# Kernel optimization log

Measured on AMD Instinct MI355X. Metric: run time of the kernel, lower is better.

Reference implementation:

```python
import jax, jax.numpy as jnp
import numpy as np


def _shift(w):
    # max(0, -min(w)): scalar shift making w + shift non-negative
    return jnp.maximum(0.0, -jnp.min(w))


def shifted_linear(x, W, b=None):
    # F.linear with non-negative weights plus row-sum correction
    alpha = _shift(W)
    y = x @ (W + alpha).T - alpha * jnp.sum(x, axis=-1, keepdims=True)
    if b is not None:
        y = y + b
    return y


def shifted_depthwise_conv(x, w, b):
    # x: (B, D, L), w: (D, 1, K) depthwise; causal-style padding K-1, sliced to L by caller
    alpha = _shift(w)
    k = w.shape[2]
    pad = k - 1
    dn = ('NCH', 'OIH', 'NCH')
    groups = w.shape[0]
    y = jax.lax.conv_general_dilated(x, w + alpha, (1,), [(pad, pad)],
                                     dimension_numbers=dn, feature_group_count=groups)
    ones_k = jnp.ones_like(w)
    ssum = jax.lax.conv_general_dilated(x, ones_k, (1,), [(pad, pad)],
                                        dimension_numbers=dn, feature_group_count=groups)
    return y - alpha * ssum + b[None, :, None]


def setup_inputs() -> dict:
    key = jax.random.key(0)
    ks = jax.random.split(key, 10)
    d_model, d_inner, d_state, d_conv, dt_rank = 1024, 2048, 16, 4, 64
    B, L = 2, 1024
    s = 0.05
    return {
        'hidden_states': jax.random.normal(ks[0], (B, L, d_model), jnp.float32),
        'W_in': jax.random.normal(ks[1], (2 * d_inner, d_model), jnp.float32) * s,
        'conv_w': jax.random.normal(ks[2], (d_inner, 1, d_conv), jnp.float32) * 0.3,
        'conv_b': jax.random.normal(ks[3], (d_inner,), jnp.float32) * s,
        'W_x': jax.random.normal(ks[4], (dt_rank + 2 * d_state, d_inner), jnp.float32) * s,
        'W_dt': jax.random.normal(ks[5], (d_inner, dt_rank), jnp.float32) * s,
        'dt_bias': jax.random.normal(ks[6], (d_inner,), jnp.float32),
        'W_out': jax.random.normal(ks[7], (d_model, d_inner), jnp.float32) * s,
        'A_log': jax.random.normal(ks[8], (d_inner, d_state), jnp.float32) * 0.5,
        'D': jax.random.normal(ks[9], (d_inner,), jnp.float32),
    }


def reference(hidden_states, W_in, conv_w, conv_b, W_x, W_dt, dt_bias, W_out, A_log, D):
    b, l, dm = hidden_states.shape
    d_inner = conv_w.shape[0]
    d_state = A_log.shape[1]
    dt_rank = W_dt.shape[1]

    A = jnp.exp(A_log)  # (d_inner, d_state), always positive

    # in_proj over (b*l, d_model) -> (b, 2*d_inner, l)
    xz = shifted_linear(hidden_states.reshape(b * l, dm), W_in)
    xz = xz.reshape(b, l, 2 * d_inner).transpose(0, 2, 1)
    x, z = xz[:, :d_inner], xz[:, d_inner:]

    # depthwise shifted conv + SiLU activation, truncated to seqlen
    x = jax.nn.silu(shifted_depthwise_conv(x, conv_w, conv_b)[..., :l])

    # x_proj -> dt_raw, B, C
    x_dbl = shifted_linear(x.transpose(0, 2, 1).reshape(b * l, d_inner), W_x)
    dt_raw = x_dbl[:, :dt_rank]
    Bm = x_dbl[:, dt_rank:dt_rank + d_state].reshape(b, l, d_state).transpose(0, 2, 1)  # (b,n,l)
    Cm = x_dbl[:, dt_rank + d_state:].reshape(b, l, d_state).transpose(0, 2, 1)         # (b,n,l)
    dt = shifted_linear(dt_raw, W_dt).reshape(b, l, d_inner).transpose(0, 2, 1)          # (b,d,l)

    # delta activation (softplus) with bias, clamped
    delta = jnp.clip(jax.nn.softplus(dt + dt_bias[None, :, None]), 1e-4, 20.0)

    # global scalar shifts for B and C
    beta = _shift(Bm)
    gamma = _shift(Cm)
    B_nn = Bm + beta
    C_nn = Cm + gamma

    # precomputed per-step operands, scan axis first: (l, b, d, n)
    deltaA = jnp.exp(-jnp.einsum('bdl,dn->lbdn', delta, A))
    dBu = jnp.einsum('bdl,bnl,bdl->lbdn', delta, B_nn, x)
    C_scan = C_nn.transpose(2, 0, 1)  # (l, b, n)

    def step(xc, inp):
        dA_i, dBu_i, C_i = inp
        xc = dA_i * xc + dBu_i                                   # (b,d,n)
        y = jnp.einsum('bdn,bn->bd', xc, C_i) - gamma * jnp.sum(xc, axis=-1)
        return xc, y

    x0 = jnp.zeros((b, d_inner, d_state), dtype=delta.dtype)
    _, ys = jax.lax.scan(step, x0, (deltaA, dBu, C_scan))        # ys: (l, b, d)

    y = ys.transpose(1, 2, 0) + x * D[None, :, None]             # (b, d, l) skip term
    y = y * jax.nn.silu(z)                                       # gate activation

    out = shifted_linear(y.transpose(0, 2, 1).reshape(b * l, d_inner), W_out)
    return out.reshape(b, l, dm)
```

## Files before the change

### kernel.cpp

```cpp
#include <hip/hip_runtime.h>
#include <hip/hip_bf16.h>
#include <math.h>

#define DM 1024
#define DI 2048
#define DS 16
#define DTR 64
#define NB 2
#define LL 1024
#define TT (NB*LL)
#define SCH 32
#define NCH (LL/SCH)
#define KPLANES 8

typedef unsigned short u16;
typedef __attribute__((ext_vector_type(8))) short bf16x8;
typedef __attribute__((ext_vector_type(4))) float f32x4;

#define LOG2E 1.4426950408889634f

__device__ inline u16 f2bf(float f) {
  union { float f; unsigned u; } c; c.f = f;
  unsigned u = c.u;
  return (u16)((u + 0x7fffu + ((u >> 16) & 1u)) >> 16);
}
__device__ inline float bf2f(u16 u) {
  union { unsigned u; float f; } c; c.u = ((unsigned)u) << 16;
  return c.f;
}

__device__ inline unsigned fkey(float f) {
  union { float f; unsigned u; } c; c.f = f;
  return (c.u & 0x80000000u) ? ~c.u : (c.u | 0x80000000u);
}
__device__ inline float funkey(unsigned k) {
  union { unsigned u; float f; } c;
  c.u = (k & 0x80000000u) ? (k & 0x7fffffffu) : ~k;
  return c.f;
}

#define GLDS16(g, l) __builtin_amdgcn_global_load_lds( \
    (const __attribute__((address_space(1))) unsigned int*)(g), \
    (__attribute__((address_space(3))) unsigned int*)(l), 16, 0, 0)

template<int BM, int BN, int EPI, int OB>
__global__ __launch_bounds__(256) void gemm_bf16(
    const u16* __restrict__ A, const u16* __restrict__ B,
    void* __restrict__ Cv, int M, int N, int K, int kpb,
    const float* __restrict__ bias) {
  constexpr int WAVES_M = BM / 64;
  constexpr int WAVES_N = 4 / WAVES_M;
  constexpr int WTM = 4;
  constexpr int WTN = BN / (WAVES_N * 16);
  constexpr int ASLABS = BM / 16;
  constexpr int SLABS = (BM + BN) / 16;
  constexpr int SPW = SLABS / 4;
  __shared__ u16 As[BM * 32];
  __shared__ u16 Bs[BN * 32];
  const int tid = threadIdx.x;
  const int wave = tid >> 6;
  const int lane = tid & 63;
  const int bm = blockIdx.y * BM;
  const int bn = blockIdx.x * BN;
  const int wm = (wave / WAVES_N) * 64;
  const int wn = (wave % WAVES_N) * (WTN * 16);
  const int r4 = lane >> 2;
  const int kc = (lane & 3) * 8;
  const int fr = lane & 15;
  const int fq = lane >> 4;
  const int koff = blockIdx.z * kpb;
  float* C = (float*)Cv + (size_t)blockIdx.z * M * N;
  u16* C16 = (u16*)Cv;

  f32x4 acc[WTM][WTN];
#pragma unroll
  for (int i = 0; i < WTM; ++i)
#pragma unroll
    for (int j = 0; j < WTN; ++j) acc[i][j] = (f32x4){0.f, 0.f, 0.f, 0.f};

  for (int k0 = koff; k0 < koff + kpb; k0 += 32) {
#pragma unroll
    for (int s = wave * SPW; s < (wave + 1) * SPW; ++s) {
      if (s < ASLABS) {
        int row = s * 16 + r4;
        GLDS16(A + (size_t)(bm + row) * K + k0 + kc, &As[s * 512]);
      } else {
        int row = (s - ASLABS) * 16 + r4;
        GLDS16(B + (size_t)(bn + row) * K + k0 + kc, &Bs[(s - ASLABS) * 512]);
      }
    }
    __syncthreads();
    bf16x8 af[WTM], bf[WTN];
#pragma unroll
    for (int i = 0; i < WTM; ++i)
      af[i] = *(const bf16x8*)&As[(wm + 16 * i + fr) * 32 + fq * 8];
#pragma unroll
    for (int j = 0; j < WTN; ++j)
      bf[j] = *(const bf16x8*)&Bs[(wn + 16 * j + fr) * 32 + fq * 8];
#pragma unroll
    for (int i = 0; i < WTM; ++i)
#pragma unroll
      for (int j = 0; j < WTN; ++j)
        acc[i][j] = __builtin_amdgcn_mfma_f32_16x16x32_bf16(af[i], bf[j], acc[i][j], 0, 0, 0);
    __syncthreads();
  }

#pragma unroll
  for (int i = 0; i < WTM; ++i) {
    int row0 = bm + wm + 16 * i + fq * 4;
#pragma unroll
    for (int j = 0; j < WTN; ++j) {
      int col = bn + wn + 16 * j + fr;
#pragma unroll
      for (int r = 0; r < 4; ++r) {
        float v = acc[i][j][r];
        if (EPI == 1) {
          v += bias[col];
          float sp = (v > 20.0f) ? v : log1pf(expf(v));
          v = fminf(fmaxf(sp, 1e-4f), 20.0f);
        }
        if (OB == 1) C16[(size_t)(row0 + r) * N + col] = f2bf(v);
        else         C[(size_t)(row0 + r) * N + col] = v;
      }
    }
  }
}

__global__ __launch_bounds__(256) void gemm3_reduce(
    const float* __restrict__ part, float* __restrict__ xdb,
    u16* __restrict__ dtraw_bf, unsigned* __restrict__ betakey) {
  int i = blockIdx.x * 256 + threadIdx.x;
  int t = i >> 7, col = i & 127;
  float s = 0.f;
#pragma unroll
  for (int z = 0; z < KPLANES; ++z) s += part[(size_t)z * TT * 128 + i];
  if (col < 96) xdb[t * 96 + col] = s;
  if (col < 64) dtraw_bf[t * 64 + col] = f2bf(s);
  float mn = (col >= 64 && col < 80) ? s : 3.4e38f;
#pragma unroll
  for (int o = 32; o; o >>= 1) mn = fminf(mn, __shfl_down(mn, o));
  __shared__ float sm[4];
  if ((threadIdx.x & 63) == 0) sm[threadIdx.x >> 6] = mn;
  __syncthreads();
  if (threadIdx.x == 0) {
    float m = fminf(fminf(sm[0], sm[1]), fminf(sm[2], sm[3]));
    atomicMin(betakey, fkey(m));
  }
}

__global__ __launch_bounds__(256) void cast_all(
    const float* __restrict__ hs, const float* __restrict__ win,
    const float* __restrict__ wout, const float* __restrict__ wx,
    const float* __restrict__ wdt,
    u16* __restrict__ hs_bf, u16* __restrict__ win_bf,
    u16* __restrict__ wout_bf, u16* __restrict__ wx_bf,
    u16* __restrict__ wdt_bf, unsigned* __restrict__ betakey) {
  int gid = blockIdx.x * 256 + threadIdx.x;
  if (gid == 0) betakey[0] = 0xFFFFFFFFu;
  const float* src; u16* dst; int off;
  if (gid < 524288)       { src = hs;   dst = hs_bf;   off = gid; }
  else if (gid < 1572864) { src = win;  dst = win_bf;  off = gid - 524288; }
  else if (gid < 2097152) { src = wout; dst = wout_bf; off = gid - 1572864; }
  else if (gid < 2146304) { src = wx;   dst = wx_bf;   off = gid - 2097152; }
  else if (gid < 2179072) { src = wdt;  dst = wdt_bf;  off = gid - 2146304; }
  else {
    ushort4 z4 = {0, 0, 0, 0};
    ((ushort4*)wx_bf)[49152 + gid - 2179072] = z4;
    return;
  }
  float4 v = ((const float4*)src)[off];
  ushort4 o;
  o.x = f2bf(v.x); o.y = f2bf(v.y); o.z = f2bf(v.z); o.w = f2bf(v.w);
  ((ushort4*)dst)[off] = o;
}

__global__ __launch_bounds__(256) void conv_silu4(
    const u16* __restrict__ xz, const float* __restrict__ w,
    const float* __restrict__ cb, u16* __restrict__ xc_bf) {
  int gid = blockIdx.x * 256 + threadIdx.x;
  int dq = (gid & 511) * 4;
  int t = gid >> 9;
  int l = t & (LL - 1);
  float wv[4][4];
#pragma unroll
  for (int j = 0; j < 4; ++j) {
    float4 ww = *(const float4*)&w[(dq + j) * 4];
    wv[j][0] = ww.x; wv[j][1] = ww.y; wv[j][2] = ww.z; wv[j][3] = ww.w;
  }
  float4 acc = *(const float4*)&cb[dq];
#pragma unroll
  for (int k = 0; k < 4; ++k) {
    int ll = l - 3 + k;
    if (ll < 0) continue;
    ushort4 xv = *(const ushort4*)&xz[(size_t)(t - 3 + k) * (2 * DI) + dq];
    acc.x += bf2f(xv.x) * wv[0][k]; acc.y += bf2f(xv.y) * wv[1][k];
    acc.z += bf2f(xv.z) * wv[2][k]; acc.w += bf2f(xv.w) * wv[3][k];
  }
  acc.x /= (1.0f + expf(-acc.x)); acc.y /= (1.0f + expf(-acc.y));
  acc.z /= (1.0f + expf(-acc.z)); acc.w /= (1.0f + expf(-acc.w));
  ushort4 o;
  o.x = f2bf(acc.x); o.y = f2bf(acc.y); o.z = f2bf(acc.z); o.w = f2bf(acc.w);
  *(ushort4*)&xc_bf[(size_t)t * DI + dq] = o;
}

__global__ __launch_bounds__(256) void scan_pass1(
    const u16* __restrict__ delta, const u16* __restrict__ xc_bf,
    const float* __restrict__ xdb, const float* __restrict__ A_log,
    const unsigned* __restrict__ betak,
    float* __restrict__ hend, float* __restrict__ Ssum) {
  const int d = blockIdx.x * 256 + threadIdx.x;
  const int c = blockIdx.y;
  const int b = blockIdx.z;
  __shared__ float Bsh[SCH][16];
  const float beta = fmaxf(0.0f, -funkey(betak[0]));
  const int t0 = b * LL + c * SCH;
  for (int i = threadIdx.x; i < SCH * 16; i += 256) {
    int tt = i >> 4, n = i & 15;
    Bsh[tt][n] = xdb[(size_t)(t0 + tt) * 96 + 64 + n] + beta;
  }
  __syncthreads();
  float Av2[16];
#pragma unroll
  for (int n = 0; n < 16; ++n) Av2[n] = expf(A_log[d * 16 + n]) * LOG2E;
  float h[16];
#pragma unroll
  for (int n = 0; n < 16; ++n) h[n] = 0.f;
  float S = 0.f;
  for (int tt = 0; tt < SCH; ++tt) {
    int t = t0 + tt;
    float dv = bf2f(delta[(size_t)t * DI + d]);
    float xv = bf2f(xc_bf[(size_t)t * DI + d]);
    float dx = dv * xv;
    S += dv;
#pragma unroll
    for (int n = 0; n < 16; ++n) {
      float a = __builtin_amdgcn_exp2f(-dv * Av2[n]);
      h[n] = a * h[n] + dx * Bsh[tt][n];
    }
  }
  size_t base = (((size_t)(b * NCH + c) * DI) + d) * 16;
#pragma unroll
  for (int n = 0; n < 16; ++n) hend[base + n] = h[n];
  Ssum[((size_t)(b * NCH + c) * DI) + d] = S;
}

__global__ __launch_bounds__(256) void scan_pass2(
    float* __restrict__ hend, const float* __restrict__ Ssum,
    const float* __restrict__ A_log) {
  int gid = blockIdx.x * 256 + threadIdx.x;
  int n = gid & 15;
  int d = (gid >> 4) & (DI - 1);
  int b = gid >> 15;
  float Av2 = expf(A_log[d * 16 + n]) * LOG2E;
  float H = 0.f;
  for (int c = 0; c < NCH; ++c) {
    size_t cb = ((size_t)(b * NCH + c) * DI) + d;
    float hl = hend[cb * 16 + n];
    float p = __builtin_amdgcn_exp2f(-Av2 * Ssum[cb]);
    hend[cb * 16 + n] = H;
    H = p * H + hl;
  }
}

__global__ __launch_bounds__(256) void scan_pass3(
    const u16* __restrict__ delta, const u16* __restrict__ xc_bf,
    const float* __restrict__ xdb, const u16* __restrict__ xz_bf,
    const float* __restrict__ A_log, const float* __restrict__ Dp,
    const unsigned* __restrict__ betak, const float* __restrict__ hstart,
    u16* __restrict__ ybf) {
  const int d = blockIdx.x * 256 + threadIdx.x;
  const int c = blockIdx.y;
  const int b = blockIdx.z;
  __shared__ float Bsh[SCH][16];
  __shared__ float Csh[SCH][16];
  const float beta = fmaxf(0.0f, -funkey(betak[0]));
  const int t0 = b * LL + c * SCH;
  for (int i = threadIdx.x; i < SCH * 16; i += 256) {
    int tt = i >> 4, n = i & 15;
    size_t row = (size_t)(t0 + tt) * 96;
    Bsh[tt][n] = xdb[row + 64 + n] + beta;
    Csh[tt][n] = xdb[row + 80 + n];
  }
  __syncthreads();
  float Av2[16];
#pragma unroll
  for (int n = 0; n < 16; ++n) Av2[n] = expf(A_log[d * 16 + n]) * LOG2E;
  float h[16];
  size_t base = (((size_t)(b * NCH + c) * DI) + d) * 16;
#pragma unroll
  for (int n = 0; n < 16; ++n) h[n] = hstart[base + n];
  const float Dd = Dp[d];
  for (int tt = 0; tt < SCH; ++tt) {
    int t = t0 + tt;
    float dv = bf2f(delta[(size_t)t * DI + d]);
    float xv = bf2f(xc_bf[(size_t)t * DI + d]);
    float dx = dv * xv;
    float yv = 0.f;
#pragma unroll
    for (int n = 0; n < 16; ++n) {
      float a = __builtin_amdgcn_exp2f(-dv * Av2[n]);
      h[n] = a * h[n] + dx * Bsh[tt][n];
      yv += h[n] * Csh[tt][n];
    }
    float zv = bf2f(xz_bf[(size_t)t * (2 * DI) + DI + d]);
    float out = (yv + xv * Dd) * (zv / (1.0f + expf(-zv)));
    ybf[(size_t)t * DI + d] = f2bf(out);
  }
}

extern "C" void kernel_launch(void* const* d_in, const int* in_sizes, int n_in,
                              void* d_out, int out_size, void* d_ws, size_t ws_size,
                              hipStream_t stream) {
  const float* hs      = (const float*)d_in[0];
  const float* W_in    = (const float*)d_in[1];
  const float* conv_w  = (const float*)d_in[2];
  const float* conv_b  = (const float*)d_in[3];
  const float* W_x     = (const float*)d_in[4];
  const float* W_dt    = (const float*)d_in[5];
  const float* dt_bias = (const float*)d_in[6];
  const float* W_out   = (const float*)d_in[7];
  const float* A_log   = (const float*)d_in[8];
  const float* Dp      = (const float*)d_in[9];
  float* out = (float*)d_out;

  float* ws       = (float*)d_ws;
  float* xz_bfR   = ws;
  float* xcv_bfR  = xz_bfR + (size_t)TT * 2 * DI / 2;
  float* xdb      = xcv_bfR + (size_t)TT * DI / 2;
  float* dlt_bfR  = xdb + (size_t)TT * 96;
  float* part     = dlt_bfR + (size_t)TT * DI / 2;
  float* betab    = part + (size_t)KPLANES * TT * 128;
  float* hend     = betab + 64;
  float* Ssum     = hend + (size_t)NB * NCH * DI * 16;
  float* hs_bfR   = Ssum + (size_t)NB * NCH * DI;
  float* win_bfR  = hs_bfR + (size_t)TT * DM / 2;
  float* wout_bfR = win_bfR + (size_t)2 * DI * DM / 2;
  float* wx_bfR   = wout_bfR + (size_t)DM * DI / 2;
  float* wdt_bfR  = wx_bfR + 131072;
  float* dtraw_bfR = wdt_bfR + 65536;

  u16* xz_bf    = (u16*)xz_bfR;
  u16* xcv_bf   = (u16*)xcv_bfR;
  u16* dlt_bf   = (u16*)dlt_bfR;
  u16* hs_bf    = (u16*)hs_bfR;
  u16* win_bf   = (u16*)win_bfR;
  u16* wout_bf  = (u16*)wout_bfR;
  u16* wx_bf    = (u16*)wx_bfR;
  u16* wdt_bf   = (u16*)wdt_bfR;
  u16* dtraw_bf = (u16*)dtraw_bfR;
  unsigned* betakey = (unsigned*)betab;
  u16* ybf      = (u16*)win_bfR;

  dim3 blk(256);

  cast_all<<<8576, blk, 0, stream>>>(hs, W_in, W_out, W_x, W_dt,
                                     hs_bf, win_bf, wout_bf, wx_bf, wdt_bf,
                                     betakey);

  gemm_bf16<128, 64, 0, 1><<<dim3(4096 / 64, TT / 128), blk, 0, stream>>>(
      hs_bf, win_bf, xz_bf, TT, 2 * DI, DM, DM, nullptr);

  conv_silu4<<<(TT * DI / 4) / 256, blk, 0, stream>>>(xz_bf, conv_w, conv_b, xcv_bf);

  gemm_bf16<64, 128, 0, 0><<<dim3(1, TT / 64, KPLANES), blk, 0, stream>>>(
      xcv_bf, wx_bf, part, TT, 128, DI, DI / KPLANES, nullptr);
  gemm3_reduce<<<1024, blk, 0, stream>>>(part, xdb, dtraw_bf, betakey);

  gemm_bf16<64, 128, 1, 1><<<dim3(DI / 128, TT / 64), blk, 0, stream>>>(
      dtraw_bf, wdt_bf, dlt_bf, TT, DI, DTR, DTR, dt_bias);

  scan_pass1<<<dim3(DI / 256, NCH, NB), blk, 0, stream>>>(
      dlt_bf, xcv_bf, xdb, A_log, betakey, hend, Ssum);
  scan_pass2<<<(NB * DI * DS) / 256, blk, 0, stream>>>(hend, Ssum, A_log);
  scan_pass3<<<dim3(DI / 256, NCH, NB), blk, 0, stream>>>(
      dlt_bf, xcv_bf, xdb, xz_bf, A_log, Dp, betakey, hend, ybf);

  gemm_bf16<64, 64, 0, 0><<<dim3(DM / 64, TT / 64), blk, 0, stream>>>(
      ybf, wout_bf, out, TT, DM, DI, DI, nullptr);
}
```

Baseline: 270.5 us.

## Replace split-K partial buffers with atomic accumulation and enlarge GEMM tiles

The x_proj split-K GEMM now atomically adds into a zeroed xdb buffer, which removes the partial-plane buffer and its reduce kernel. A small dtbeta kernel replaces the reduce and handles the dt bf16 cast and the beta min. The in_proj GEMM moves to 128x128 tiles. The out_proj GEMM becomes a 4-way split-K with 128x128 tiles that atomically accumulates into the output, which cast_all now zeroes. The atomics add contention, make float summation order nondeterministic, and cut the number of blocks for in_proj.

```diff
diff --git a/kernel.cpp b/kernel.cpp
--- a/kernel.cpp
+++ b/kernel.cpp
@@ -11,7 +11,6 @@
 #define TT (NB*LL)
 #define SCH 32
 #define NCH (LL/SCH)
-#define KPLANES 8
 
 typedef unsigned short u16;
 typedef __attribute__((ext_vector_type(8))) short bf16x8;
@@ -43,7 +42,7 @@
     (const __attribute__((address_space(1))) unsigned int*)(g), \
     (__attribute__((address_space(3))) unsigned int*)(l), 16, 0, 0)
 
-template<int BM, int BN, int EPI, int OB>
+template<int BM, int BN, int EPI, int OB, int CG = 0>
 __global__ __launch_bounds__(256) void gemm_bf16(
     const u16* __restrict__ A, const u16* __restrict__ B,
     void* __restrict__ Cv, int M, int N, int K, int kpb,
@@ -69,7 +68,7 @@
   const int fr = lane & 15;
   const int fq = lane >> 4;
   const int koff = blockIdx.z * kpb;
-  float* C = (float*)Cv + (size_t)blockIdx.z * M * N;
+  float* C = (float*)Cv + (OB == 0 ? (size_t)blockIdx.z * M * N : (size_t)0);
   u16* C16 = (u16*)Cv;
 
   f32x4 acc[WTM][WTN];
@@ -119,30 +118,43 @@
           float sp = (v > 20.0f) ? v : log1pf(expf(v));
           v = fminf(fmaxf(sp, 1e-4f), 20.0f);
         }
-        if (OB == 1) C16[(size_t)(row0 + r) * N + col] = f2bf(v);
-        else         C[(size_t)(row0 + r) * N + col] = v;
+        if (OB == 1) {
+          C16[(size_t)(row0 + r) * N + col] = f2bf(v);
+        } else if (OB == 2) {
+          if (CG == 0 || col < CG) {
+            const int ldc = (CG > 0) ? CG : N;
+            atomicAdd(&C[(size_t)(row0 + r) * ldc + col], v);
+          }
+        } else {
+          C[(size_t)(row0 + r) * N + col] = v;
+        }
       }
     }
   }
 }
 
-__global__ __launch_bounds__(256) void gemm3_reduce(
-    const float* __restrict__ part, float* __restrict__ xdb,
-    u16* __restrict__ dtraw_bf, unsigned* __restrict__ betakey) {
-  int i = blockIdx.x * 256 + threadIdx.x;
-  int t = i >> 7, col = i & 127;
-  float s = 0.f;
-#pragma unroll
-  for (int z = 0; z < KPLANES; ++z) s += part[(size_t)z * TT * 128 + i];
-  if (col < 96) xdb[t * 96 + col] = s;
-  if (col < 64) dtraw_bf[t * 64 + col] = f2bf(s);
-  float mn = (col >= 64 && col < 80) ? s : 3.4e38f;
+__global__ __launch_bounds__(256) void dtbeta(
+    const float* __restrict__ xdb, u16* __restrict__ dtraw_bf,
+    unsigned* __restrict__ betakey) {
+  const int t0 = blockIdx.x * 32;
+  const int tid = threadIdx.x;
+#pragma unroll
+  for (int i = tid; i < 32 * 64; i += 256) {
+    int t = t0 + (i >> 6), c = i & 63;
+    dtraw_bf[t * 64 + c] = f2bf(xdb[t * 96 + c]);
+  }
+  float mn = 3.4e38f;
+#pragma unroll
+  for (int i = tid; i < 32 * 16; i += 256) {
+    int t = t0 + (i >> 4), n = i & 15;
+    mn = fminf(mn, xdb[t * 96 + 64 + n]);
+  }
 #pragma unroll
   for (int o = 32; o; o >>= 1) mn = fminf(mn, __shfl_down(mn, o));
   __shared__ float sm[4];
-  if ((threadIdx.x & 63) == 0) sm[threadIdx.x >> 6] = mn;
+  if ((tid & 63) == 0) sm[tid >> 6] = mn;
   __syncthreads();
-  if (threadIdx.x == 0) {
+  if (tid == 0) {
     float m = fminf(fminf(sm[0], sm[1]), fminf(sm[2], sm[3]));
     atomicMin(betakey, fkey(m));
   }
@@ -154,7 +166,8 @@
     const float* __restrict__ wdt,
     u16* __restrict__ hs_bf, u16* __restrict__ win_bf,
     u16* __restrict__ wout_bf, u16* __restrict__ wx_bf,
-    u16* __restrict__ wdt_bf, unsigned* __restrict__ betakey) {
+    u16* __restrict__ wdt_bf, float* __restrict__ xdb,
+    float* __restrict__ outz, unsigned* __restrict__ betakey) {
   int gid = blockIdx.x * 256 + threadIdx.x;
   if (gid == 0) betakey[0] = 0xFFFFFFFFu;
   const float* src; u16* dst; int off;
@@ -163,9 +176,17 @@
   else if (gid < 2097152) { src = wout; dst = wout_bf; off = gid - 1572864; }
   else if (gid < 2146304) { src = wx;   dst = wx_bf;   off = gid - 2097152; }
   else if (gid < 2179072) { src = wdt;  dst = wdt_bf;  off = gid - 2146304; }
-  else {
+  else if (gid < 2195456) {
     ushort4 z4 = {0, 0, 0, 0};
     ((ushort4*)wx_bf)[49152 + gid - 2179072] = z4;
+    return;
+  } else if (gid < 2244608) {
+    float4 z = {0.f, 0.f, 0.f, 0.f};
+    ((float4*)xdb)[gid - 2195456] = z;
+    return;
+  } else {
+    float4 z = {0.f, 0.f, 0.f, 0.f};
+    ((float4*)outz)[gid - 2244608] = z;
     return;
   }
   float4 v = ((const float4*)src)[off];
@@ -328,8 +349,7 @@
   float* xcv_bfR  = xz_bfR + (size_t)TT * 2 * DI / 2;
   float* xdb      = xcv_bfR + (size_t)TT * DI / 2;
   float* dlt_bfR  = xdb + (size_t)TT * 96;
-  float* part     = dlt_bfR + (size_t)TT * DI / 2;
-  float* betab    = part + (size_t)KPLANES * TT * 128;
+  float* betab    = dlt_bfR + (size_t)TT * DI / 2;
   float* hend     = betab + 64;
   float* Ssum     = hend + (size_t)NB * NCH * DI * 16;
   float* hs_bfR   = Ssum + (size_t)NB * NCH * DI;
@@ -353,18 +373,19 @@
 
   dim3 blk(256);
 
-  cast_all<<<8576, blk, 0, stream>>>(hs, W_in, W_out, W_x, W_dt,
-                                     hs_bf, win_bf, wout_bf, wx_bf, wdt_bf,
-                                     betakey);
-
-  gemm_bf16<128, 64, 0, 1><<<dim3(4096 / 64, TT / 128), blk, 0, stream>>>(
+  cast_all<<<10816, blk, 0, stream>>>(hs, W_in, W_out, W_x, W_dt,
+                                      hs_bf, win_bf, wout_bf, wx_bf, wdt_bf,
+                                      xdb, out, betakey);
+
+  gemm_bf16<128, 128, 0, 1><<<dim3(4096 / 128, TT / 128), blk, 0, stream>>>(
       hs_bf, win_bf, xz_bf, TT, 2 * DI, DM, DM, nullptr);
 
   conv_silu4<<<(TT * DI / 4) / 256, blk, 0, stream>>>(xz_bf, conv_w, conv_b, xcv_bf);
 
-  gemm_bf16<64, 128, 0, 0><<<dim3(1, TT / 64, KPLANES), blk, 0, stream>>>(
-      xcv_bf, wx_bf, part, TT, 128, DI, DI / KPLANES, nullptr);
-  gemm3_reduce<<<1024, blk, 0, stream>>>(part, xdb, dtraw_bf, betakey);
+  gemm_bf16<64, 128, 0, 2, 96><<<dim3(1, TT / 64, 8), blk, 0, stream>>>(
+      xcv_bf, wx_bf, xdb, TT, 128, DI, DI / 8, nullptr);
+
+  dtbeta<<<64, blk, 0, stream>>>(xdb, dtraw_bf, betakey);
 
   gemm_bf16<64, 128, 1, 1><<<dim3(DI / 128, TT / 64), blk, 0, stream>>>(
       dtraw_bf, wdt_bf, dlt_bf, TT, DI, DTR, DTR, dt_bias);
@@ -375,6 +396,6 @@
   scan_pass3<<<dim3(DI / 256, NCH, NB), blk, 0, stream>>>(
       dlt_bf, xcv_bf, xdb, xz_bf, A_log, Dp, betakey, hend, ybf);
 
-  gemm_bf16<64, 64, 0, 0><<<dim3(DM / 64, TT / 64), blk, 0, stream>>>(
-      ybf, wout_bf, out, TT, DM, DI, DI, nullptr);
-}
+  gemm_bf16<128, 128, 0, 2, 0><<<dim3(DM / 128, TT / 128, 4), blk, 0, stream>>>(
+      ybf, wout_bf, out, TT, DM, DI, DI / 4, nullptr);
+}
```

New measurement: 264.0 us. 2.4% less time.
